# Performance work log

Hardware: AMD Instinct MI355X
Metric: run time of the kernel (lower is better)

Reference implementation:

```python
import jax, jax.numpy as jnp
import numpy as np

N = 100000
E = 1000000
F_IN = 128
H = 64
C = 40


def _glorot(key, shape):
    fan_in, fan_out = shape[1], shape[0]
    lim = float(np.sqrt(6.0 / (fan_in + fan_out)))
    return jax.random.uniform(key, shape, jnp.float32, -lim, lim)


def setup_inputs() -> dict:
    key = jax.random.key(0)
    ks = jax.random.split(key, 8)
    x = jax.random.normal(ks[0], (N, F_IN), jnp.float32)
    edge_index = jax.random.randint(ks[1], (2, E), 0, N, jnp.int64)
    params = {
        # conv1: lin(F_IN->H), outer1(H->H), outer2(H->H)
        "w1_lin": _glorot(ks[2], (H, F_IN)), "b1_lin": jnp.zeros((H,), jnp.float32),
        "w1_o1": _glorot(ks[3], (H, H)), "b1_o1": jnp.zeros((H,), jnp.float32),
        "w1_o2": _glorot(ks[4], (H, H)), "b1_o2": jnp.zeros((H,), jnp.float32),
        # conv2: lin(H->C), outer1(C->C), outer2(C->C)
        "w2_lin": _glorot(ks[5], (C, H)), "b2_lin": jnp.zeros((C,), jnp.float32),
        "w2_o1": _glorot(ks[6], (C, C)), "b2_o1": jnp.zeros((C,), jnp.float32),
        "w2_o2": _glorot(ks[7], (C, C)), "b2_o2": jnp.zeros((C,), jnp.float32),
    }
    return {"x": x, "edge_index": edge_index, **params}


def gcn_conv(x, src, dst, w_lin, b_lin, w_o1, b_o1, w_o2, b_o2):
    # x: [N, Fin] -> lin -> [N, Fout]
    h = x @ w_lin.T + b_lin
    # propagate: gather h[src] ([E, Fout]) and scatter-add into dst;
    # self-loops (i -> i) are equivalent to adding h itself.
    agg = jax.ops.segment_sum(h[src], dst, num_segments=h.shape[0]) + h
    out = jax.nn.relu(agg)
    out = jax.nn.relu(out @ w_o1.T + b_o1)
    return out @ w_o2.T + b_o2


def reference(x, edge_index, w1_lin, b1_lin, w1_o1, b1_o1, w1_o2, b1_o2,
              w2_lin, b2_lin, w2_o1, b2_o1, w2_o2, b2_o2):
    src, dst = edge_index[0], edge_index[1]
    h = gcn_conv(x, src, dst, w1_lin, b1_lin, w1_o1, b1_o1, w1_o2, b1_o2)
    h = jax.nn.relu(h)
    # dropout is identity in eval mode (training=False)
    return gcn_conv(h, src, dst, w2_lin, b2_lin, w2_o1, b2_o1, w2_o2, b2_o2)
```

## Files before the change

### kernel.cpp

```cpp
#include <hip/hip_runtime.h>

static constexpr int FIN = 128;
static constexpr int HD  = 64;
static constexpr int CD  = 40;
static constexpr int S2  = 48;

typedef __attribute__((ext_vector_type(8))) short short8;
typedef __attribute__((ext_vector_type(4))) float f32x4;

__device__ __forceinline__ unsigned short f2b(float f)
{
    union { float f; unsigned u; } x; x.f = f;
    unsigned u = x.u;
    return (unsigned short)((u + 0x7FFF + ((u >> 16) & 1)) >> 16);
}
__device__ __forceinline__ float b2f(unsigned short b)
{
    union { unsigned u; float f; } x; x.u = ((unsigned)b) << 16;
    return x.f;
}

static constexpr int NBMAX = 512;
static constexpr int ACH   = 4096;

__global__ __launch_bounds__(256)
void prep_kernel(const float* __restrict__ w1_lin, const float* __restrict__ w1_o1,
                 const float* __restrict__ w1_o2, const float* __restrict__ w2_lin,
                 const float* __restrict__ w2_o1, const float* __restrict__ w2_o2,
                 unsigned short* __restrict__ wb, int* __restrict__ bucketCount)
{
    int i = blockIdx.x * 256 + threadIdx.x;
    if (i < NBMAX) bucketCount[i] = 0;
    if (i >= 25600) return;
    const float* src; int Kin, Kp, Oin, off;
    if (i < 8192)       { src = w1_lin; Kin = 128; Kp = 128; Oin = 64; off = 0; }
    else if (i < 12288) { src = w1_o1;  Kin = 64;  Kp = 64;  Oin = 64; off = 8192; }
    else if (i < 16384) { src = w1_o2;  Kin = 64;  Kp = 64;  Oin = 64; off = 12288; }
    else if (i < 19456) { src = w2_lin; Kin = 64;  Kp = 64;  Oin = 40; off = 16384; }
    else if (i < 22528) { src = w2_o1;  Kin = 40;  Kp = 64;  Oin = 40; off = 19456; }
    else                { src = w2_o2;  Kin = 40;  Kp = 64;  Oin = 40; off = 22528; }
    int j = i - off;
    int o = j / Kp, k = j - o * Kp;
    float v = (o < Oin && k < Kin) ? src[o * Kin + k] : 0.f;
    wb[i] = f2b(v);
}

template<int NKT, int NOT>
__device__ __forceinline__ void mfma_tile(const short8* a, const unsigned short* __restrict__ Wbf,
                                          int l16, int quad, f32x4* acc)
{
    constexpr int KP = NKT * 32;
#pragma unroll
    for (int ot = 0; ot < NOT; ++ot) {
        acc[ot] = (f32x4){0.f, 0.f, 0.f, 0.f};
        const unsigned short* Wrow = Wbf + (size_t)(ot * 16 + l16) * KP + quad * 8;
#pragma unroll
        for (int kt = 0; kt < NKT; ++kt) {
            short8 b = *reinterpret_cast<const short8*>(Wrow + kt * 32);
            acc[ot] = __builtin_amdgcn_mfma_f32_16x16x32_bf16(a[kt], b, acc[ot], 0, 0, 0);
        }
    }
}

__device__ __forceinline__ short8 relu_bf16x8(short8 v)
{
#pragma unroll
    for (int j = 0; j < 8; ++j) {
        unsigned short u = (unsigned short)v[j];
        if (u & 0x8000) v[j] = 0;
    }
    return v;
}

__global__ __launch_bounds__(256)
void mv1_bhist_kernel(const float* __restrict__ x, const unsigned short* __restrict__ wb1_lin,
                      const float* __restrict__ b1_lin, unsigned short* __restrict__ h,
                      int n, int tgrid,
                      const int* __restrict__ dst, int* __restrict__ bucketCount, int e, int nb)
{
    __shared__ int cnt[NBMAX];
    if (blockIdx.x >= tgrid) {
        const int bb = blockIdx.x - tgrid;
        const int t = threadIdx.x;
        for (int j = t; j < nb; j += 256) cnt[j] = 0;
        __syncthreads();
        const int i0 = bb * ACH;
        const int i1 = min(e, i0 + ACH);
        for (int i = i0 + t; i < i1; i += 256)
            atomicAdd(&cnt[dst[i] >> 8], 1);
        __syncthreads();
        for (int j = t; j < nb; j += 256)
            if (cnt[j]) atomicAdd(&bucketCount[j], cnt[j]);
        return;
    }
    const int t = threadIdx.x, wave = t >> 6, lane = t & 63;
    const int quad = lane >> 4, l16 = lane & 15;
    const int n0 = blockIdx.x * 64, m0 = wave * 16;
    int row = n0 + m0 + l16; if (row >= n) row = n - 1;

    short8 a[4];
#pragma unroll
    for (int kt = 0; kt < 4; ++kt) {
        const float* p = x + (size_t)row * FIN + kt * 32 + quad * 8;
        float4 f0 = *reinterpret_cast<const float4*>(p);
        float4 f1 = *reinterpret_cast<const float4*>(p + 4);
        short8 v;
        v[0] = (short)f2b(f0.x); v[1] = (short)f2b(f0.y);
        v[2] = (short)f2b(f0.z); v[3] = (short)f2b(f0.w);
        v[4] = (short)f2b(f1.x); v[5] = (short)f2b(f1.y);
        v[6] = (short)f2b(f1.z); v[7] = (short)f2b(f1.w);
        a[kt] = v;
    }
    f32x4 acc[4];
    mfma_tile<4, 4>(a, wb1_lin, l16, quad, acc);
#pragma unroll
    for (int ot = 0; ot < 4; ++ot) {
        int o = ot * 16 + l16;
        float bv = b1_lin[o];
#pragma unroll
        for (int r = 0; r < 4; ++r) {
            int node = n0 + m0 + quad * 4 + r;
            if (node < n) h[(size_t)node * HD + o] = f2b(acc[ot][r] + bv);
        }
    }
}

__global__ __launch_bounds__(256)
void chainB_kernel(const unsigned short* __restrict__ agg,
                   const unsigned short* __restrict__ wo1, const float* __restrict__ bo1,
                   const unsigned short* __restrict__ wo2, const float* __restrict__ bo2,
                   const unsigned short* __restrict__ wlin, const float* __restrict__ blin,
                   unsigned short* __restrict__ out, int n)
{
    constexpr int KS = 72;
    __shared__ unsigned short lds[64 * KS];
    const int t = threadIdx.x, wave = t >> 6, lane = t & 63;
    const int quad = lane >> 4, l16 = lane & 15;
    const int n0 = blockIdx.x * 64, m0 = wave * 16;
    int row = n0 + m0 + l16; if (row >= n) row = n - 1;

    short8 a[2];
#pragma unroll
    for (int kt = 0; kt < 2; ++kt) {
        short8 v = *reinterpret_cast<const short8*>(agg + (size_t)row * HD + kt * 32 + quad * 8);
        a[kt] = relu_bf16x8(v);
    }

    f32x4 acc[4];
    mfma_tile<2, 4>(a, wo1, l16, quad, acc);
#pragma unroll
    for (int ot = 0; ot < 4; ++ot) {
        int o = ot * 16 + l16;
        float bv = bo1[o];
#pragma unroll
        for (int r = 0; r < 4; ++r) {
            float v = fmaxf(acc[ot][r] + bv, 0.f);
            lds[(m0 + quad * 4 + r) * KS + o] = f2b(v);
        }
    }
#pragma unroll
    for (int kt = 0; kt < 2; ++kt)
        a[kt] = *reinterpret_cast<const short8*>(&lds[(m0 + l16) * KS + kt * 32 + quad * 8]);

    mfma_tile<2, 4>(a, wo2, l16, quad, acc);
#pragma unroll
    for (int ot = 0; ot < 4; ++ot) {
        int o = ot * 16 + l16;
        float bv = bo2[o];
#pragma unroll
        for (int r = 0; r < 4; ++r) {
            float v = fmaxf(acc[ot][r] + bv, 0.f);
            lds[(m0 + quad * 4 + r) * KS + o] = f2b(v);
        }
    }
#pragma unroll
    for (int kt = 0; kt < 2; ++kt)
        a[kt] = *reinterpret_cast<const short8*>(&lds[(m0 + l16) * KS + kt * 32 + quad * 8]);

    f32x4 acc3[3];
    mfma_tile<2, 3>(a, wlin, l16, quad, acc3);
#pragma unroll
    for (int ot = 0; ot < 3; ++ot) {
        int o = ot * 16 + l16;
        float bv = (o < CD) ? blin[o] : 0.f;
#pragma unroll
        for (int r = 0; r < 4; ++r) {
            int node = n0 + m0 + quad * 4 + r;
            if (node < n) {
                float v = (o < CD) ? (acc3[ot][r] + bv) : 0.f;
                out[(size_t)node * S2 + o] = f2b(v);
            }
        }
    }
}

__global__ __launch_bounds__(256)
void chainC_kernel(const unsigned short* __restrict__ agg,
                   const unsigned short* __restrict__ wo1, const float* __restrict__ bo1,
                   const unsigned short* __restrict__ wo2, const float* __restrict__ bo2,
                   float* __restrict__ out, int n)
{
    constexpr int KS = 72;
    __shared__ unsigned short lds[64 * KS];
    const int t = threadIdx.x, wave = t >> 6, lane = t & 63;
    const int quad = lane >> 4, l16 = lane & 15;
    const int n0 = blockIdx.x * 64, m0 = wave * 16;

    for (int i = lane; i < 16 * 16; i += 64) {
        int rr = i >> 4, cc = i & 15;
        lds[(m0 + rr) * KS + 48 + cc] = 0;
    }

    int row = n0 + m0 + l16; if (row >= n) row = n - 1;
    short8 a[2];
    {
        short8 v = *reinterpret_cast<const short8*>(agg + (size_t)row * S2 + quad * 8);
        a[0] = relu_bf16x8(v);
    }
    {
        short8 v = {0, 0, 0, 0, 0, 0, 0, 0};
        if (quad == 0) {
            v = *reinterpret_cast<const short8*>(agg + (size_t)row * S2 + 32);
            v = relu_bf16x8(v);
        }
        a[1] = v;
    }

    f32x4 acc[3];
    mfma_tile<2, 3>(a, wo1, l16, quad, acc);
#pragma unroll
    for (int ot = 0; ot < 3; ++ot) {
        int o = ot * 16 + l16;
        float bv = (o < CD) ? bo1[o] : 0.f;
#pragma unroll
        for (int r = 0; r < 4; ++r) {
            float v = (o < CD) ? fmaxf(acc[ot][r] + bv, 0.f) : 0.f;
            lds[(m0 + quad * 4 + r) * KS + o] = f2b(v);
        }
    }
#pragma unroll
    for (int kt = 0; kt < 2; ++kt)
        a[kt] = *reinterpret_cast<const short8*>(&lds[(m0 + l16) * KS + kt * 32 + quad * 8]);

    mfma_tile<2, 3>(a, wo2, l16, quad, acc);
#pragma unroll
    for (int ot = 0; ot < 3; ++ot) {
        int o = ot * 16 + l16;
        if (o < CD) {
            float bv = bo2[o];
#pragma unroll
            for (int r = 0; r < 4; ++r) {
                int node = n0 + m0 + quad * 4 + r;
                if (node < n) out[(size_t)node * CD + o] = acc[ot][r] + bv;
            }
        }
    }
}

__global__ __launch_bounds__(256)
void bscan_kernel(const int* __restrict__ bucketCount, int* __restrict__ bucketOff,
                  int* __restrict__ bucketCursor, int nb)
{
    __shared__ int sA[NBMAX], sB[NBMAX];
    const int t = threadIdx.x;
#pragma unroll
    for (int s = t; s < NBMAX; s += 256) sA[s] = (s < nb) ? bucketCount[s] : 0;
    __syncthreads();
    int* pa = sA; int* pb = sB;
    for (int off = 1; off < NBMAX; off <<= 1) {
#pragma unroll
        for (int s = t; s < NBMAX; s += 256)
            pb[s] = pa[s] + ((s >= off) ? pa[s - off] : 0);
        __syncthreads();
        int* tmp = pa; pa = pb; pb = tmp;
    }
#pragma unroll
    for (int s = t; s <= nb && s < NBMAX; s += 256) {
        int v = (s == 0) ? 0 : pa[s - 1];
        bucketOff[s] = v;
        if (s < nb) bucketCursor[s] = v;
    }
}

__global__ __launch_bounds__(256)
void bpart_kernel(const int* __restrict__ src, const int* __restrict__ dst,
                  int* __restrict__ bucketCursor, uint2* __restrict__ pairs,
                  int e, int nb)
{
    __shared__ int cnt[NBMAX];
    __shared__ int base[NBMAX];
    const int t = threadIdx.x;
    for (int j = t; j < nb; j += 256) cnt[j] = 0;
    __syncthreads();
    const int i0 = blockIdx.x * ACH;
    const int i1 = min(e, i0 + ACH);
    for (int i = i0 + t; i < i1; i += 256)
        atomicAdd(&cnt[dst[i] >> 8], 1);
    __syncthreads();
    for (int j = t; j < nb; j += 256) {
        int c = cnt[j];
        base[j] = c ? atomicAdd(&bucketCursor[j], c) : 0;
        cnt[j] = 0;
    }
    __syncthreads();
    for (int i = i0 + t; i < i1; i += 256) {
        int d = dst[i];
        int bkt = d >> 8;
        int pos = base[bkt] + atomicAdd(&cnt[bkt], 1);
        pairs[pos] = make_uint2((unsigned)d, (unsigned)src[i]);
    }
}

__global__ __launch_bounds__(256)
void bbuild_kernel(const uint2* __restrict__ pairs, const int* __restrict__ bucketOff,
                   int* __restrict__ rowptr_end, int* __restrict__ deg_g,
                   int* __restrict__ eidx, int n)
{
    __shared__ int deg[256], sA[256], sB[256], cur[256];
    const int t = threadIdx.x;
    const int b = blockIdx.x;
    const int node0 = b << 8;
    const int e0 = bucketOff[b], e1 = bucketOff[b + 1];

    deg[t] = 0;
    __syncthreads();
    for (int i = e0 + t; i < e1; i += 256)
        atomicAdd(&deg[pairs[i].x & 255], 1);
    __syncthreads();
    sA[t] = deg[t];
    __syncthreads();
    int* pa = sA; int* pb = sB;
    for (int off = 1; off < 256; off <<= 1) {
        pb[t] = pa[t] + ((t >= off) ? pa[t - off] : 0);
        __syncthreads();
        int* tmp = pa; pa = pb; pb = tmp;
    }
    const int node = node0 + t;
    if (node < n) {
        rowptr_end[node] = e0 + pa[t];
        deg_g[node] = deg[t];
    }
    cur[t] = pa[t] - deg[t];
    __syncthreads();
    for (int i = e0 + t; i < e1; i += 256) {
        uint2 p = pairs[i];
        int pos = e0 + atomicAdd(&cur[p.x & 255], 1);
        eidx[pos] = (int)p.y;
    }
}

template<int STRIDE, int CHUNKS>
__global__ __launch_bounds__(256)
void gatherw_kernel(const int* __restrict__ rowptr_end, const int* __restrict__ deg_g,
                    const int* __restrict__ eidx, const unsigned short* __restrict__ h,
                    unsigned short* __restrict__ agg, int n)
{
    const int wave = threadIdx.x >> 6, lane = threadIdx.x & 63;
    const int ec = lane >> 3;
    const int ch = lane & 7;
    const int node = blockIdx.x * 4 + wave;
    if (node >= n) return;

    const bool chact = (ch < CHUNKS);
    float a[8] = {0.f, 0.f, 0.f, 0.f, 0.f, 0.f, 0.f, 0.f};

    if (ec == 0 && chact) {
        union { uint4 u; unsigned short s[8]; } v;
        v.u = *reinterpret_cast<const uint4*>(h + (size_t)node * STRIDE + ch * 8);
#pragma unroll
        for (int j = 0; j < 8; ++j) a[j] = b2f(v.s[j]);
    }

    const int end   = rowptr_end[node];
    const int start = end - deg_g[node];

    for (int base = start; base < end; base += 16) {
        const int i0 = base + ec, i1 = base + 8 + ec;
        const bool v0 = (i0 < end) && chact;
        const bool v1 = (i1 < end) && chact;
        union { uint4 u; unsigned short s[8]; } u0, u1;
        if (v0) {
            int s = eidx[i0];
            u0.u = *reinterpret_cast<const uint4*>(h + (size_t)s * STRIDE + ch * 8);
        }
        if (v1) {
            int s = eidx[i1];
            u1.u = *reinterpret_cast<const uint4*>(h + (size_t)s * STRIDE + ch * 8);
        }
        if (v0) {
#pragma unroll
            for (int j = 0; j < 8; ++j) a[j] += b2f(u0.s[j]);
        }
        if (v1) {
#pragma unroll
            for (int j = 0; j < 8; ++j) a[j] += b2f(u1.s[j]);
        }
    }

#pragma unroll
    for (int j = 0; j < 8; ++j) {
        a[j] += __shfl_xor(a[j], 8, 64);
        a[j] += __shfl_xor(a[j], 16, 64);
        a[j] += __shfl_xor(a[j], 32, 64);
    }

    if (ec == 0 && chact) {
        union { uint4 u; unsigned short s[8]; } o;
#pragma unroll
        for (int j = 0; j < 8; ++j) o.s[j] = f2b(a[j]);
        *reinterpret_cast<uint4*>(agg + (size_t)node * STRIDE + ch * 8) = o.u;
    }
}

extern "C" void kernel_launch(void* const* d_in, const int* in_sizes, int n_in,
                              void* d_out, int out_size, void* d_ws, size_t ws_size,
                              hipStream_t stream)
{
    const float* x      = (const float*)d_in[0];
    const int*   ei     = (const int*)d_in[1];
    const float* w1_lin = (const float*)d_in[2];
    const float* b1_lin = (const float*)d_in[3];
    const float* w1_o1  = (const float*)d_in[4];
    const float* b1_o1  = (const float*)d_in[5];
    const float* w1_o2  = (const float*)d_in[6];
    const float* b1_o2  = (const float*)d_in[7];
    const float* w2_lin = (const float*)d_in[8];
    const float* b2_lin = (const float*)d_in[9];
    const float* w2_o1  = (const float*)d_in[10];
    const float* b2_o1  = (const float*)d_in[11];
    const float* w2_o2  = (const float*)d_in[12];
    const float* b2_o2  = (const float*)d_in[13];

    const int n = in_sizes[0] / FIN;
    const int e = in_sizes[1] / 2;
    const int* src = ei;
    const int* dst = ei + e;

    unsigned short* ws0 = (unsigned short*)d_ws;
    unsigned short* ws1 = ws0 + (size_t)n * HD;
    unsigned short* wb  = ws1 + (size_t)n * HD;
    unsigned short* wb1_lin = wb;
    unsigned short* wb1_o1  = wb1_lin + 64 * 128;
    unsigned short* wb1_o2  = wb1_o1  + 64 * 64;
    unsigned short* wb2_lin = wb1_o2  + 64 * 64;
    unsigned short* wb2_o1  = wb2_lin + 48 * 64;
    unsigned short* wb2_o2  = wb2_o1  + 48 * 64;
    uint2* pairs        = (uint2*)(wb2_o2 + 48 * 64);
    int*   bucketCount  = (int*)(pairs + e);
    int*   bucketOff    = bucketCount + NBMAX;
    int*   bucketCursor = bucketOff + NBMAX + 1;
    float* outp = (float*)d_out;

    int* eidx   = (int*)d_out;
    int* deg    = eidx + e;
    int* rowptr = deg + n;

    const int nb    = (n + 255) >> 8;
    const int agrid = (e + ACH - 1) / ACH;
    const int tgrid = (n + 63) / 64;
    const int wgrid = (n + 3) / 4;

    prep_kernel<<<(25600 + 255) / 256, 256, 0, stream>>>(
        w1_lin, w1_o1, w1_o2, w2_lin, w2_o1, w2_o2, wb, bucketCount);

    mv1_bhist_kernel<<<tgrid + agrid, 256, 0, stream>>>(
        x, wb1_lin, b1_lin, ws0, n, tgrid, dst, bucketCount, e, nb);

    bscan_kernel<<<1, 256, 0, stream>>>(bucketCount, bucketOff, bucketCursor, nb);
    bpart_kernel<<<agrid, 256, 0, stream>>>(src, dst, bucketCursor, pairs, e, nb);
    bbuild_kernel<<<nb, 256, 0, stream>>>(pairs, bucketOff, rowptr, deg, eidx, n);

    gatherw_kernel<HD, 8><<<wgrid, 256, 0, stream>>>(rowptr, deg, eidx, ws0, ws1, n);

    chainB_kernel<<<tgrid, 256, 0, stream>>>(
        ws1, wb1_o1, b1_o1, wb1_o2, b1_o2, wb2_lin, b2_lin, ws0, n);

    gatherw_kernel<S2, 6><<<wgrid, 256, 0, stream>>>(rowptr, deg, eidx, ws0, ws1, n);

    chainC_kernel<<<tgrid, 256, 0, stream>>>(
        ws1, wb2_o1, b2_o1, wb2_o2, b2_o2, outp, n);
}
```

Baseline: 295.7 us.

## Replace CSR build and per-node gather with bucketed shared-memory atomic aggregation

Drops the per-bucket CSR build kernel and aggregates neighbours straight from the dst-bucketed (dst,src) pair list. Each block owns 128 destination nodes and accumulates their rows in fp32 shared memory using shared atomics, seeded with the self-loop term. Bucket width is halved to 128 nodes and NBMAX doubled to match. This removes one kernel and the eidx/rowptr writes and reads, at the cost of shared-memory atomic contention, a non-deterministic summation order, and only about 782 blocks for each gather.

After: 958.7 us. +224.2%, slower.

```diff
diff --git a/kernel.cpp b/kernel.cpp
--- a/kernel.cpp
+++ b/kernel.cpp
@@ -20,7 +20,7 @@
     return x.f;
 }
 
-static constexpr int NBMAX = 512;
+static constexpr int NBMAX = 1024;
 static constexpr int ACH   = 4096;
 
 __global__ __launch_bounds__(256)
@@ -87,7 +87,7 @@
         const int i0 = bb * ACH;
         const int i1 = min(e, i0 + ACH);
         for (int i = i0 + t; i < i1; i += 256)
-            atomicAdd(&cnt[dst[i] >> 8], 1);
+            atomicAdd(&cnt[dst[i] >> 7], 1);
         __syncthreads();
         for (int j = t; j < nb; j += 256)
             if (cnt[j]) atomicAdd(&bucketCount[j], cnt[j]);
@@ -295,7 +295,7 @@
     const int i0 = blockIdx.x * ACH;
     const int i1 = min(e, i0 + ACH);
     for (int i = i0 + t; i < i1; i += 256)
-        atomicAdd(&cnt[dst[i] >> 8], 1);
+        atomicAdd(&cnt[dst[i] >> 7], 1);
     __syncthreads();
     for (int j = t; j < nb; j += 256) {
         int c = cnt[j];
@@ -305,110 +305,62 @@
     __syncthreads();
     for (int i = i0 + t; i < i1; i += 256) {
         int d = dst[i];
-        int bkt = d >> 8;
+        int bkt = d >> 7;
         int pos = base[bkt] + atomicAdd(&cnt[bkt], 1);
         pairs[pos] = make_uint2((unsigned)d, (unsigned)src[i]);
     }
 }
 
-__global__ __launch_bounds__(256)
-void bbuild_kernel(const uint2* __restrict__ pairs, const int* __restrict__ bucketOff,
-                   int* __restrict__ rowptr_end, int* __restrict__ deg_g,
-                   int* __restrict__ eidx, int n)
-{
-    __shared__ int deg[256], sA[256], sB[256], cur[256];
+template<int SL, int SLP, int CHUNKS>
+__global__ __launch_bounds__(256)
+void bgather_kernel(const uint2* __restrict__ pairs, const int* __restrict__ bucketOff,
+                    const unsigned short* __restrict__ h, unsigned short* __restrict__ agg,
+                    int n)
+{
+    __shared__ float acc[128 * SLP];
     const int t = threadIdx.x;
     const int b = blockIdx.x;
-    const int node0 = b << 8;
+    const int node0 = b << 7;
+    constexpr int V8 = SL / 8;
+
+    for (int idx = t; idx < 128 * V8; idx += 256) {
+        int row = idx / V8, c8 = idx - row * V8;
+        int gn = node0 + row;
+        union { uint4 u; unsigned short s[8]; } v;
+        if (gn < n) v.u = *reinterpret_cast<const uint4*>(h + (size_t)gn * SL + c8 * 8);
+        else        v.u = make_uint4(0u, 0u, 0u, 0u);
+        float* a = &acc[row * SLP + c8 * 8];
+#pragma unroll
+        for (int j = 0; j < 8; ++j) a[j] = b2f(v.s[j]);
+    }
+    __syncthreads();
+
     const int e0 = bucketOff[b], e1 = bucketOff[b + 1];
-
-    deg[t] = 0;
-    __syncthreads();
-    for (int i = e0 + t; i < e1; i += 256)
-        atomicAdd(&deg[pairs[i].x & 255], 1);
-    __syncthreads();
-    sA[t] = deg[t];
-    __syncthreads();
-    int* pa = sA; int* pb = sB;
-    for (int off = 1; off < 256; off <<= 1) {
-        pb[t] = pa[t] + ((t >= off) ? pa[t - off] : 0);
-        __syncthreads();
-        int* tmp = pa; pa = pb; pb = tmp;
-    }
-    const int node = node0 + t;
-    if (node < n) {
-        rowptr_end[node] = e0 + pa[t];
-        deg_g[node] = deg[t];
-    }
-    cur[t] = pa[t] - deg[t];
-    __syncthreads();
-    for (int i = e0 + t; i < e1; i += 256) {
-        uint2 p = pairs[i];
-        int pos = e0 + atomicAdd(&cur[p.x & 255], 1);
-        eidx[pos] = (int)p.y;
-    }
-}
-
-template<int STRIDE, int CHUNKS>
-__global__ __launch_bounds__(256)
-void gatherw_kernel(const int* __restrict__ rowptr_end, const int* __restrict__ deg_g,
-                    const int* __restrict__ eidx, const unsigned short* __restrict__ h,
-                    unsigned short* __restrict__ agg, int n)
-{
-    const int wave = threadIdx.x >> 6, lane = threadIdx.x & 63;
-    const int ec = lane >> 3;
-    const int ch = lane & 7;
-    const int node = blockIdx.x * 4 + wave;
-    if (node >= n) return;
-
-    const bool chact = (ch < CHUNKS);
-    float a[8] = {0.f, 0.f, 0.f, 0.f, 0.f, 0.f, 0.f, 0.f};
-
-    if (ec == 0 && chact) {
-        union { uint4 u; unsigned short s[8]; } v;
-        v.u = *reinterpret_cast<const uint4*>(h + (size_t)node * STRIDE + ch * 8);
-#pragma unroll
-        for (int j = 0; j < 8; ++j) a[j] = b2f(v.s[j]);
-    }
-
-    const int end   = rowptr_end[node];
-    const int start = end - deg_g[node];
-
-    for (int base = start; base < end; base += 16) {
-        const int i0 = base + ec, i1 = base + 8 + ec;
-        const bool v0 = (i0 < end) && chact;
-        const bool v1 = (i1 < end) && chact;
-        union { uint4 u; unsigned short s[8]; } u0, u1;
-        if (v0) {
-            int s = eidx[i0];
-            u0.u = *reinterpret_cast<const uint4*>(h + (size_t)s * STRIDE + ch * 8);
-        }
-        if (v1) {
-            int s = eidx[i1];
-            u1.u = *reinterpret_cast<const uint4*>(h + (size_t)s * STRIDE + ch * 8);
-        }
-        if (v0) {
-#pragma unroll
-            for (int j = 0; j < 8; ++j) a[j] += b2f(u0.s[j]);
-        }
-        if (v1) {
-#pragma unroll
-            for (int j = 0; j < 8; ++j) a[j] += b2f(u1.s[j]);
-        }
-    }
-
-#pragma unroll
-    for (int j = 0; j < 8; ++j) {
-        a[j] += __shfl_xor(a[j], 8, 64);
-        a[j] += __shfl_xor(a[j], 16, 64);
-        a[j] += __shfl_xor(a[j], 32, 64);
-    }
-
-    if (ec == 0 && chact) {
-        union { uint4 u; unsigned short s[8]; } o;
-#pragma unroll
-        for (int j = 0; j < 8; ++j) o.s[j] = f2b(a[j]);
-        *reinterpret_cast<uint4*>(agg + (size_t)node * STRIDE + ch * 8) = o.u;
+    const int ec = t >> 3, ch = t & 7;
+    if (ch < CHUNKS) {
+#pragma unroll 4
+        for (int i = e0 + ec; i < e1; i += 32) {
+            uint2 p = pairs[i];
+            int dl = (int)(p.x & 127);
+            union { uint4 u; unsigned short s[8]; } v;
+            v.u = *reinterpret_cast<const uint4*>(h + (size_t)p.y * SL + ch * 8);
+            float* a = &acc[dl * SLP + ch * 8];
+#pragma unroll
+            for (int j = 0; j < 8; ++j) atomicAdd(&a[j], b2f(v.s[j]));
+        }
+    }
+    __syncthreads();
+
+    for (int idx = t; idx < 128 * V8; idx += 256) {
+        int row = idx / V8, c8 = idx - row * V8;
+        int gn = node0 + row;
+        if (gn < n) {
+            const float* a = &acc[row * SLP + c8 * 8];
+            union { uint4 u; unsigned short s[8]; } o;
+#pragma unroll
+            for (int j = 0; j < 8; ++j) o.s[j] = f2b(a[j]);
+            *reinterpret_cast<uint4*>(agg + (size_t)gn * SL + c8 * 8) = o.u;
+        }
     }
 }
 
@@ -451,14 +403,9 @@
     int*   bucketCursor = bucketOff + NBMAX + 1;
     float* outp = (float*)d_out;
 
-    int* eidx   = (int*)d_out;
-    int* deg    = eidx + e;
-    int* rowptr = deg + n;
-
-    const int nb    = (n + 255) >> 8;
+    const int nb    = (n + 127) >> 7;
     const int agrid = (e + ACH - 1) / ACH;
     const int tgrid = (n + 63) / 64;
-    const int wgrid = (n + 3) / 4;
 
     prep_kernel<<<(25600 + 255) / 256, 256, 0, stream>>>(
         w1_lin, w1_o1, w1_o2, w2_lin, w2_o1, w2_o2, wb, bucketCount);
@@ -468,14 +415,13 @@
 
     bscan_kernel<<<1, 256, 0, stream>>>(bucketCount, bucketOff, bucketCursor, nb);
     bpart_kernel<<<agrid, 256, 0, stream>>>(src, dst, bucketCursor, pairs, e, nb);
-    bbuild_kernel<<<nb, 256, 0, stream>>>(pairs, bucketOff, rowptr, deg, eidx, n);
-
-    gatherw_kernel<HD, 8><<<wgrid, 256, 0, stream>>>(rowptr, deg, eidx, ws0, ws1, n);
+
+    bgather_kernel<HD, HD + 4, 8><<<nb, 256, 0, stream>>>(pairs, bucketOff, ws0, ws1, n);
 
     chainB_kernel<<<tgrid, 256, 0, stream>>>(
         ws1, wb1_o1, b1_o1, wb1_o2, b1_o2, wb2_lin, b2_lin, ws0, n);
 
-    gatherw_kernel<S2, 6><<<wgrid, 256, 0, stream>>>(rowptr, deg, eidx, ws0, ws1, n);
+    bgather_kernel<S2, S2 + 4, 6><<<nb, 256, 0, stream>>>(pairs, bucketOff, ws0, ws1, n);
 
     chainC_kernel<<<tgrid, 256, 0, stream>>>(
         ws1, wb2_o1, b2_o1, wb2_o2, b2_o2, outp, n);
```
